# Optimization experiments

Measured on AMD Instinct MI355X. Metric: run time of the kernel, lower is better.

Reference implementation:

```python
import jax, jax.numpy as jnp
import numpy as np

B, T, E = 16, 1024, 1024
H, Dh = 16, 64


def setup_inputs() -> dict:
    key = jax.random.key(0)
    ks = jax.random.split(key, 6)
    s = 1.0 / np.sqrt(E)
    x = jax.random.normal(ks[0], (B, T, E), dtype=jnp.float32)
    Wq = jax.random.uniform(ks[1], (H, E, Dh), minval=-s, maxval=s, dtype=jnp.float32)
    Wk = jax.random.uniform(ks[2], (H, E, Dh), minval=-s, maxval=s, dtype=jnp.float32)
    Wv = jax.random.uniform(ks[3], (H, E, Dh), minval=-s, maxval=s, dtype=jnp.float32)
    sp = 1.0 / np.sqrt(H * Dh)
    Wo = jax.random.uniform(ks[4], (H * Dh, E), minval=-sp, maxval=sp, dtype=jnp.float32)
    bo = jax.random.uniform(ks[5], (E,), minval=-sp, maxval=sp, dtype=jnp.float32)
    return {"x": x, "Wq": Wq, "Wk": Wk, "Wv": Wv, "Wo": Wo, "bo": bo}


def reference(x, Wq, Wk, Wv, Wo, bo):
    # batched per-head projections: [B,T,E] x [H,E,Dh] -> [B,H,T,Dh]
    q = jnp.einsum('bte,hed->bhtd', x, Wq)
    k = jnp.einsum('bte,hed->bhtd', x, Wk)
    v = jnp.einsum('bte,hed->bhtd', x, Wv)
    scale = 1.0 / np.sqrt(Dh).astype(np.float32)
    wei = jnp.einsum('bhtd,bhsd->bhts', q, k) * scale  # [B,H,T,T]
    causal = jnp.tril(jnp.ones((T, T), dtype=bool))
    wei = jnp.where(causal, wei, -jnp.inf)
    wei = jax.nn.softmax(wei, axis=-1)
    out = jnp.einsum('bhts,bhsd->bhtd', wei, v)  # [B,H,T,Dh]
    out = out.transpose(0, 2, 1, 3).reshape(B, T, H * Dh)  # concat heads
    return out @ Wo + bo
```

## Files before the change

### kernel.cpp

```cpp
#include <hip/hip_runtime.h>
#include <stdint.h>

typedef __attribute__((ext_vector_type(8))) short short8;
typedef __attribute__((ext_vector_type(4))) float f32x4;
typedef __attribute__((ext_vector_type(4))) unsigned short u16x4;

#define DEVI static __device__ __forceinline__

DEVI unsigned short f2bf(float f) {
  unsigned int u = __builtin_bit_cast(unsigned int, f);
  u += 0x7fffu + ((u >> 16) & 1u);
  return (unsigned short)(u >> 16);
}

DEVI void glds16(const void* g, void* lds_uniform) {
  typedef const __attribute__((address_space(1))) unsigned int* gp_t;
  typedef __attribute__((address_space(3))) unsigned int* lp_t;
  __builtin_amdgcn_global_load_lds((gp_t)(uintptr_t)g, (lp_t)(uintptr_t)lds_uniform, 16, 0, 0);
}


__global__ __launch_bounds__(256) void cvt_x_kernel(const float* __restrict__ in,
                                                    unsigned short* __restrict__ out, int n4) {
  typedef __attribute__((ext_vector_type(4))) float f4;
  typedef __attribute__((ext_vector_type(4))) unsigned short u4;
  const f4* in4 = (const f4*)in;
  u4* out4 = (u4*)out;
  for (int i = blockIdx.x * blockDim.x + threadIdx.x; i < n4; i += gridDim.x * blockDim.x) {
    f4 v = in4[i];
    u4 o;
    o[0] = f2bf(v[0]); o[1] = f2bf(v[1]); o[2] = f2bf(v[2]); o[3] = f2bf(v[3]);
    out4[i] = o;
  }
}

__global__ __launch_bounds__(256) void cvt_w_kernel(const float* __restrict__ in,
                                                    unsigned short* __restrict__ out,
                                                    int total, int log2C) {
  int i = blockIdx.x * blockDim.x + threadIdx.x;
  if (i >= total) return;
  int r = i & 1023;
  int rest = i >> 10;
  int c = rest & ((1 << log2C) - 1);
  int b = rest >> log2C;
  out[i] = f2bf(in[((((size_t)b << 10) | (size_t)r) << log2C) | (size_t)c]);
}

template <int MODE>
__global__ __launch_bounds__(256)
void gemm128(const unsigned short* __restrict__ A,
             const unsigned short* __restrict__ Bt,
             unsigned short* __restrict__ OutB,
             float* __restrict__ OutF,
             const float* __restrict__ bias) {
  __shared__ unsigned short As[128 * 64];
  __shared__ unsigned short Bs[128 * 64];
  const int tid = threadIdx.x;
  const int w = tid >> 6, lane = tid & 63;
  const int l15 = lane & 15, l4 = lane >> 4;

  const int SN = (MODE == 0) ? 6 : 2;
  const int q8 = (MODE == 0) ? 384 : 128;
  const int phys = blockIdx.x;
  const int wgid = (phys & 7) * q8 + (phys >> 3);
  const int st = wgid >> 4, loc = wgid & 15;
  const int sm = st / SN, sn = st % SN;
  const int bm = (((sm << 2) + (loc >> 2)) << 7);
  const int bn = (((sn << 2) + (loc & 3)) << 7);

  f32x4 acc[4][4];
#pragma unroll
  for (int i = 0; i < 4; ++i)
#pragma unroll
    for (int j = 0; j < 4; ++j) acc[i][j] = f32x4{0.f, 0.f, 0.f, 0.f};

  const int wr = w >> 1, wc = w & 1;

  int Crow[4], Kel[4];
#pragma unroll
  for (int j = 0; j < 4; ++j) {
    int C = (((j << 2) + w) << 6) + lane;
    int row = C >> 3, cc = C & 7;
    Crow[j] = row;
    Kel[j] = ((cc ^ (row & 7)) << 3);
  }

  for (int kt = 0; kt < 16; ++kt) {
    int k0 = kt << 6;
#pragma unroll
    for (int j = 0; j < 4; ++j) {
      const unsigned short* g = A + (size_t)(bm + Crow[j]) * 1024 + k0 + Kel[j];
      glds16(g, &As[(size_t)(((j << 2) + w) << 6) * 8]);
    }
#pragma unroll
    for (int j = 0; j < 4; ++j) {
      const unsigned short* g = Bt + (size_t)(bn + Crow[j]) * 1024 + k0 + Kel[j];
      glds16(g, &Bs[(size_t)(((j << 2) + w) << 6) * 8]);
    }
    __syncthreads();
    __builtin_amdgcn_s_setprio(1);
#pragma unroll
    for (int ks = 0; ks < 2; ++ks) {
      short8 af[4], bfr[4];
#pragma unroll
      for (int mi = 0; mi < 4; ++mi) {
        int row = (wr << 6) + (mi << 4) + l15;
        int ch = ((ks << 2) + l4) ^ (row & 7);
        af[mi] = *(const short8*)&As[(row << 6) + (ch << 3)];
      }
#pragma unroll
      for (int ni = 0; ni < 4; ++ni) {
        int row = (wc << 6) + (ni << 4) + l15;
        int ch = ((ks << 2) + l4) ^ (row & 7);
        bfr[ni] = *(const short8*)&Bs[(row << 6) + (ch << 3)];
      }
#pragma unroll
      for (int mi = 0; mi < 4; ++mi)
#pragma unroll
        for (int ni = 0; ni < 4; ++ni)
          acc[mi][ni] = __builtin_amdgcn_mfma_f32_16x16x32_bf16(af[mi], bfr[ni], acc[mi][ni], 0, 0, 0);
    }
    __builtin_amdgcn_s_setprio(0);
    __syncthreads();
  }

  if (MODE == 0) {
    const int nb = bn + (wc << 6);
    const int z = nb >> 10;
    if (z < 2) {
      unsigned short* Oz = OutB + (size_t)z * 16777216;
#pragma unroll
      for (int mi = 0; mi < 4; ++mi) {
#pragma unroll
        for (int r = 0; r < 4; ++r) {
          int m = bm + (wr << 6) + (mi << 4) + (l4 << 2) + r;
          int b = m >> 10, t = m & 1023;
#pragma unroll
          for (int ni = 0; ni < 4; ++ni) {
            int n1 = (nb + (ni << 4) + l15) & 1023;
            int h = n1 >> 6, d = n1 & 63;
            Oz[((size_t)(b * 16 + h) * 1024 + t) * 64 + d] = f2bf(acc[mi][ni][r]);
          }
        }
      }
    } else {
      unsigned short* Oz = OutB + (size_t)2 * 16777216;
#pragma unroll
      for (int mi = 0; mi < 4; ++mi) {
        int tb = bm + (wr << 6) + (mi << 4) + (l4 << 2);
        int bb = tb >> 10, tt = tb & 1023;
#pragma unroll
        for (int ni = 0; ni < 4; ++ni) {
          int n1 = (nb + (ni << 4) + l15) & 1023;
          int hh = n1 >> 6, dd = n1 & 63;
          u16x4 pk;
#pragma unroll
          for (int r = 0; r < 4; ++r) pk[r] = f2bf(acc[mi][ni][r]);
          *(u16x4*)&Oz[(((size_t)((bb << 4) + hh) << 6) + (size_t)dd) * 1024 + tt] = pk;
        }
      }
    }
  } else {
#pragma unroll
    for (int mi = 0; mi < 4; ++mi) {
#pragma unroll
      for (int r = 0; r < 4; ++r) {
        int m = bm + (wr << 6) + (mi << 4) + (l4 << 2) + r;
#pragma unroll
        for (int ni = 0; ni < 4; ++ni) {
          int n = bn + (wc << 6) + (ni << 4) + l15;
          OutF[(size_t)m * 1024 + n] = acc[mi][ni][r] + bias[n];
        }
      }
    }
  }
}

__global__ __launch_bounds__(256)
void attn_fa(const unsigned short* __restrict__ Qb,
             const unsigned short* __restrict__ Kb,
             const unsigned short* __restrict__ Vtb,
             unsigned short* __restrict__ Ob) {
  __shared__ unsigned short Ks[2][64 * 64];
  __shared__ unsigned short Vs[2][64 * 64];
  __shared__ unsigned short Ps[4][16 * 64];
  const int tid = threadIdx.x, w = tid >> 6, lane = tid & 63;
  const int l15 = lane & 15, l4 = lane >> 4;
  const int phys = blockIdx.x;
  const int ord = phys >> 3;
  const int bx = ord & 7;
  const int bh = ((phys & 7) << 5) | (ord >> 3);
  const unsigned short* Q = Qb + ((size_t)bh << 16);
  const unsigned short* K = Kb + ((size_t)bh << 16);
  const unsigned short* Vt = Vtb + ((size_t)bh << 16);
  const int b = bh >> 4, h = bh & 15;
  const float SC = 0.125f * 1.44269504088896340736f;
  const float NEGINF = -__builtin_inff();

  int srow[2], skoff[2];
#pragma unroll
  for (int c = 0; c < 2; ++c) {
    int C = (c << 8) + tid;
    int row = C >> 3, cc = C & 7;
    srow[c] = row;
    skoff[c] = ((cc ^ (row & 7)) << 3);
  }
  const int sdst = (w << 6) << 3;

  for (int ph = 0; ph < 2; ++ph) {
    const int qidx = ph ? bx : (15 - bx);
    const int q0 = qidx << 6;
    const int nt = qidx + 1;
    const int qrow = q0 + (w << 4) + l15;

    short8 bq0, bq1;
    {
      const unsigned short* qp = Q + (size_t)qrow * 64 + (l4 << 3);
      bq0 = *(const short8*)qp;
      bq1 = *(const short8*)(qp + 32);
    }

    f32x4 o[4];
#pragma unroll
    for (int nf = 0; nf < 4; ++nf) o[nf] = f32x4{0.f, 0.f, 0.f, 0.f};
    float mreg = NEGINF, lreg = 0.f;

#pragma unroll
    for (int c = 0; c < 2; ++c) {
      glds16(K + (size_t)(srow[c] << 6) + skoff[c], &Ks[0][(c << 11) + sdst]);
      glds16(Vt + (size_t)(srow[c] << 10) + skoff[c], &Vs[0][(c << 11) + sdst]);
    }
    __syncthreads();

    for (int it = 0; it < nt; ++it) {
      const int cur = it & 1;
      if (it + 1 < nt) {
        const int kv0n = (it + 1) << 6;
#pragma unroll
        for (int c = 0; c < 2; ++c) {
          glds16(K + (size_t)((kv0n + srow[c]) << 6) + skoff[c], &Ks[cur ^ 1][(c << 11) + sdst]);
          glds16(Vt + (size_t)(srow[c] << 10) + kv0n + skoff[c], &Vs[cur ^ 1][(c << 11) + sdst]);
        }
      }

      f32x4 s[4];
      __builtin_amdgcn_s_setprio(1);
#pragma unroll
      for (int n = 0; n < 4; ++n) {
        const int row = (n << 4) + l15;
        const int rb = row << 6;
        short8 ak0 = *(const short8*)&Ks[cur][rb + ((l4 ^ (row & 7)) << 3)];
        short8 ak1 = *(const short8*)&Ks[cur][rb + (((4 + l4) ^ (row & 7)) << 3)];
        f32x4 a = f32x4{0.f, 0.f, 0.f, 0.f};
        a = __builtin_amdgcn_mfma_f32_16x16x32_bf16(ak0, bq0, a, 0, 0, 0);
        a = __builtin_amdgcn_mfma_f32_16x16x32_bf16(ak1, bq1, a, 0, 0, 0);
        s[n] = a;
      }
      __builtin_amdgcn_s_setprio(0);

      const int kv0 = it << 6;
      const bool diag = (it == nt - 1);
      float p[4][4];
      float mx = NEGINF;
#pragma unroll
      for (int n = 0; n < 4; ++n)
#pragma unroll
        for (int r = 0; r < 4; ++r) {
          float v = s[n][r] * SC;
          if (diag) {
            int kvg = kv0 + (n << 4) + (l4 << 2) + r;
            v = (kvg <= qrow) ? v : NEGINF;
          }
          p[n][r] = v;
          mx = fmaxf(mx, v);
        }
      mx = fmaxf(mx, __shfl_xor(mx, 16));
      mx = fmaxf(mx, __shfl_xor(mx, 32));
      float mnew = fmaxf(mreg, mx);
      float alpha = exp2f(mreg - mnew);
      mreg = mnew;
      float rs = 0.f;
#pragma unroll
      for (int n = 0; n < 4; ++n)
#pragma unroll
        for (int r = 0; r < 4; ++r) {
          float pv = exp2f(p[n][r] - mreg);
          p[n][r] = pv;
          rs += pv;
        }
      rs += __shfl_xor(rs, 16);
      rs += __shfl_xor(rs, 32);
      lreg = lreg * alpha + rs;

      float a_r[4];
#pragma unroll
      for (int r = 0; r < 4; ++r)
        a_r[r] = __shfl(alpha, (lane & 0x30) | ((l4 << 2) | r));
#pragma unroll
      for (int nf = 0; nf < 4; ++nf)
#pragma unroll
        for (int r = 0; r < 4; ++r) o[nf][r] *= a_r[r];

#pragma unroll
      for (int n = 0; n < 4; ++n) {
        u16x4 pk;
#pragma unroll
        for (int r = 0; r < 4; ++r) pk[r] = f2bf(p[n][r]);
        const int kc = (n << 1) + (l4 >> 1);
        char* addr = (char*)&Ps[w][0] + (l15 << 7) + ((kc ^ (l15 & 7)) << 4) + ((l4 & 1) << 3);
        *(u16x4*)addr = pk;
      }

      short8 pa0 = *(const short8*)((char*)&Ps[w][0] + (l15 << 7) + ((l4 ^ (l15 & 7)) << 4));
      short8 pa1 = *(const short8*)((char*)&Ps[w][0] + (l15 << 7) + (((4 + l4) ^ (l15 & 7)) << 4));
      __builtin_amdgcn_s_setprio(1);
#pragma unroll
      for (int nf = 0; nf < 4; ++nf) {
        const int drow = (nf << 4) + l15;
        const int db = drow << 6;
        short8 vb0 = *(const short8*)&Vs[cur][db + ((l4 ^ (drow & 7)) << 3)];
        short8 vb1 = *(const short8*)&Vs[cur][db + (((4 + l4) ^ (drow & 7)) << 3)];
        o[nf] = __builtin_amdgcn_mfma_f32_16x16x32_bf16(pa0, vb0, o[nf], 0, 0, 0);
        o[nf] = __builtin_amdgcn_mfma_f32_16x16x32_bf16(pa1, vb1, o[nf], 0, 0, 0);
      }
      __builtin_amdgcn_s_setprio(0);
      __syncthreads();
    }

    float linv = 1.0f / lreg;
    float l_r[4];
#pragma unroll
    for (int r = 0; r < 4; ++r)
      l_r[r] = __shfl(linv, (lane & 0x30) | ((l4 << 2) | r));
#pragma unroll
    for (int r = 0; r < 4; ++r) {
      const int t = q0 + (w << 4) + (l4 << 2) + r;
      size_t base = ((size_t)(b * 1024 + t) << 10) + (h << 6);
#pragma unroll
      for (int nf = 0; nf < 4; ++nf)
        Ob[base + (nf << 4) + l15] = f2bf(o[nf][r] * l_r[r]);
    }
  }
}


extern "C" void kernel_launch(void* const* d_in, const int* in_sizes, int n_in,
                              void* d_out, int out_size, void* d_ws, size_t ws_size,
                              hipStream_t stream) {
  const float* x  = (const float*)d_in[0];
  const float* Wq = (const float*)d_in[1];
  const float* Wk = (const float*)d_in[2];
  const float* Wv = (const float*)d_in[3];
  const float* Wo = (const float*)d_in[4];
  const float* bo = (const float*)d_in[5];
  float* out = (float*)d_out;

  unsigned char* ws = (unsigned char*)d_ws;
  unsigned short* xb  = (unsigned short*)(ws);
  unsigned short* wT  = (unsigned short*)(ws + 33554432);
  unsigned short* woT = (unsigned short*)(ws + 33554432 + 6291456);
  unsigned short* qkv = (unsigned short*)(ws + 41943040);
  unsigned short* Ob  = xb;

  cvt_x_kernel<<<2048, 256, 0, stream>>>(x, xb, 4194304);
  cvt_w_kernel<<<4096, 256, 0, stream>>>(Wq, wT,              1 << 20, 6);
  cvt_w_kernel<<<4096, 256, 0, stream>>>(Wk, wT + (1 << 20),  1 << 20, 6);
  cvt_w_kernel<<<4096, 256, 0, stream>>>(Wv, wT + (2 << 20),  1 << 20, 6);
  cvt_w_kernel<<<4096, 256, 0, stream>>>(Wo, woT,             1 << 20, 10);

  gemm128<0><<<3072, 256, 0, stream>>>(xb, wT, qkv, nullptr, nullptr);
  attn_fa<<<2048, 256, 0, stream>>>(qkv, qkv + 16777216, qkv + 33554432, Ob);
  gemm128<1><<<1024, 256, 0, stream>>>(Ob, woT, nullptr, out, bo);
}
```

Before: 418.9 us.

## Switch projection GEMMs to 256x256 tiles with double-buffered LDS pipeline

Replaces the 128x128, 256-thread GEMM with a 256x256, 512-thread kernel that double-buffers A/B tiles in LDS and overlaps the global-to-LDS load for the next k-step with MFMA compute, using explicit vmcnt waits and barriers. Each wave now computes a 128x64 sub-tile in four quadrant passes, which raises reuse per loaded byte and halves the number of workgroups. It also merges the three Q/K/V weight conversion launches into one kernel. The cost is much more LDS per block (128 KB), higher register pressure from 32 accumulators, and fewer blocks for MODE 1 (256), which may underfill the GPU.

```diff
diff --git a/kernel.cpp b/kernel.cpp
--- a/kernel.cpp
+++ b/kernel.cpp
@@ -34,6 +34,19 @@
   }
 }
 
+__global__ __launch_bounds__(256) void cvt_w3_kernel(const float* __restrict__ Wq,
+                                                     const float* __restrict__ Wk,
+                                                     const float* __restrict__ Wv,
+                                                     unsigned short* __restrict__ out) {
+  int i = blockIdx.x * blockDim.x + threadIdx.x;
+  int z = i >> 20, loc = i & 1048575;
+  const float* W = (z == 0) ? Wq : ((z == 1) ? Wk : Wv);
+  int r = loc & 1023;
+  int rest = loc >> 10;
+  int c = rest & 63, hh = rest >> 6;
+  out[i] = f2bf(W[((((size_t)hh << 10) | (size_t)r) << 6) | (size_t)c]);
+}
+
 __global__ __launch_bounds__(256) void cvt_w_kernel(const float* __restrict__ in,
                                                     unsigned short* __restrict__ out,
                                                     int total, int log2C) {
@@ -47,93 +60,115 @@
 }
 
 template <int MODE>
-__global__ __launch_bounds__(256)
-void gemm128(const unsigned short* __restrict__ A,
+__global__ __launch_bounds__(512, 2)
+void gemm256(const unsigned short* __restrict__ A,
              const unsigned short* __restrict__ Bt,
              unsigned short* __restrict__ OutB,
              float* __restrict__ OutF,
              const float* __restrict__ bias) {
-  __shared__ unsigned short As[128 * 64];
-  __shared__ unsigned short Bs[128 * 64];
+  __shared__ unsigned short As[2][256 * 64];
+  __shared__ unsigned short Bs[2][256 * 64];
   const int tid = threadIdx.x;
   const int w = tid >> 6, lane = tid & 63;
   const int l15 = lane & 15, l4 = lane >> 4;
-
-  const int SN = (MODE == 0) ? 6 : 2;
-  const int q8 = (MODE == 0) ? 384 : 128;
+  const int wm = w >> 2, wn = w & 3;
+
   const int phys = blockIdx.x;
-  const int wgid = (phys & 7) * q8 + (phys >> 3);
-  const int st = wgid >> 4, loc = wgid & 15;
-  const int sm = st / SN, sn = st % SN;
-  const int bm = (((sm << 2) + (loc >> 2)) << 7);
-  const int bn = (((sn << 2) + (loc & 3)) << 7);
-
-  f32x4 acc[4][4];
-#pragma unroll
-  for (int i = 0; i < 4; ++i)
+  const int wgid = (MODE == 0) ? ((phys & 7) * 96 + (phys >> 3))
+                               : ((phys & 7) * 32 + (phys >> 3));
+  const int sm = (MODE == 0) ? (wgid / 12) : (wgid >> 2);
+  const int sn = (MODE == 0) ? (wgid % 12) : (wgid & 3);
+  const int bm = sm << 8, bn = sn << 8;
+
+  int srow[4], skoff[4];
+#pragma unroll
+  for (int j = 0; j < 4; ++j) {
+    int C = (j << 9) + tid;
+    srow[j] = C >> 3;
+    skoff[j] = (((C & 7) ^ (srow[j] & 7)) << 3);
+  }
+
+  f32x4 acc[8][4];
+#pragma unroll
+  for (int i = 0; i < 8; ++i)
 #pragma unroll
     for (int j = 0; j < 4; ++j) acc[i][j] = f32x4{0.f, 0.f, 0.f, 0.f};
 
-  const int wr = w >> 1, wc = w & 1;
-
-  int Crow[4], Kel[4];
-#pragma unroll
-  for (int j = 0; j < 4; ++j) {
-    int C = (((j << 2) + w) << 6) + lane;
-    int row = C >> 3, cc = C & 7;
-    Crow[j] = row;
-    Kel[j] = ((cc ^ (row & 7)) << 3);
-  }
+  auto stage = [&](int buf, int kt) {
+    const int k0 = kt << 6;
+#pragma unroll
+    for (int j = 0; j < 4; ++j)
+      glds16(A + (size_t)(bm + srow[j]) * 1024 + k0 + skoff[j],
+             &As[buf][((j << 9) + (w << 6)) << 3]);
+#pragma unroll
+    for (int j = 0; j < 4; ++j)
+      glds16(Bt + (size_t)(bn + srow[j]) * 1024 + k0 + skoff[j],
+             &Bs[buf][((j << 9) + (w << 6)) << 3]);
+  };
+
+  stage(0, 0);
+  stage(1, 1);
+  asm volatile("s_waitcnt vmcnt(8)" ::: "memory");
+  __builtin_amdgcn_s_barrier();
+  __builtin_amdgcn_sched_barrier(0);
 
   for (int kt = 0; kt < 16; ++kt) {
-    int k0 = kt << 6;
-#pragma unroll
-    for (int j = 0; j < 4; ++j) {
-      const unsigned short* g = A + (size_t)(bm + Crow[j]) * 1024 + k0 + Kel[j];
-      glds16(g, &As[(size_t)(((j << 2) + w) << 6) * 8]);
-    }
-#pragma unroll
-    for (int j = 0; j < 4; ++j) {
-      const unsigned short* g = Bt + (size_t)(bn + Crow[j]) * 1024 + k0 + Kel[j];
-      glds16(g, &Bs[(size_t)(((j << 2) + w) << 6) * 8]);
-    }
-    __syncthreads();
-    __builtin_amdgcn_s_setprio(1);
-#pragma unroll
-    for (int ks = 0; ks < 2; ++ks) {
-      short8 af[4], bfr[4];
-#pragma unroll
-      for (int mi = 0; mi < 4; ++mi) {
-        int row = (wr << 6) + (mi << 4) + l15;
-        int ch = ((ks << 2) + l4) ^ (row & 7);
-        af[mi] = *(const short8*)&As[(row << 6) + (ch << 3)];
-      }
-#pragma unroll
-      for (int ni = 0; ni < 4; ++ni) {
-        int row = (wc << 6) + (ni << 4) + l15;
-        int ch = ((ks << 2) + l4) ^ (row & 7);
-        bfr[ni] = *(const short8*)&Bs[(row << 6) + (ch << 3)];
-      }
-#pragma unroll
-      for (int mi = 0; mi < 4; ++mi)
-#pragma unroll
-        for (int ni = 0; ni < 4; ++ni)
-          acc[mi][ni] = __builtin_amdgcn_mfma_f32_16x16x32_bf16(af[mi], bfr[ni], acc[mi][ni], 0, 0, 0);
-    }
-    __builtin_amdgcn_s_setprio(0);
-    __syncthreads();
+    const int cur = kt & 1;
+    if (kt >= 1) {
+      if (kt < 15) {
+        stage(cur ^ 1, kt + 1);
+        asm volatile("s_waitcnt vmcnt(8)" ::: "memory");
+      } else {
+        asm volatile("s_waitcnt vmcnt(0)" ::: "memory");
+      }
+      __builtin_amdgcn_s_barrier();
+      __builtin_amdgcn_sched_barrier(0);
+    }
+#pragma unroll
+    for (int q = 0; q < 4; ++q) {
+      const int qr = q >> 1, qc = q & 1;
+      short8 af[4][2], bfr[2][2];
+#pragma unroll
+      for (int ri = 0; ri < 4; ++ri)
+#pragma unroll
+        for (int ks = 0; ks < 2; ++ks) {
+          int row = (wm << 7) + (qr << 6) + (ri << 4) + l15;
+          int ch = ((ks << 2) + l4) ^ (row & 7);
+          af[ri][ks] = *(const short8*)&As[cur][(row << 6) + (ch << 3)];
+        }
+#pragma unroll
+      for (int ni = 0; ni < 2; ++ni)
+#pragma unroll
+        for (int ks = 0; ks < 2; ++ks) {
+          int row = (wn << 6) + (qc << 5) + (ni << 4) + l15;
+          int ch = ((ks << 2) + l4) ^ (row & 7);
+          bfr[ni][ks] = *(const short8*)&Bs[cur][(row << 6) + (ch << 3)];
+        }
+      __builtin_amdgcn_s_barrier();
+      __builtin_amdgcn_s_setprio(1);
+#pragma unroll
+      for (int ks = 0; ks < 2; ++ks)
+#pragma unroll
+        for (int ri = 0; ri < 4; ++ri)
+#pragma unroll
+          for (int ni = 0; ni < 2; ++ni)
+            acc[(qr << 2) + ri][(qc << 1) + ni] = __builtin_amdgcn_mfma_f32_16x16x32_bf16(
+                af[ri][ks], bfr[ni][ks], acc[(qr << 2) + ri][(qc << 1) + ni], 0, 0, 0);
+      __builtin_amdgcn_s_setprio(0);
+      __builtin_amdgcn_s_barrier();
+    }
   }
 
   if (MODE == 0) {
-    const int nb = bn + (wc << 6);
+    const int nb = bn + (wn << 6);
     const int z = nb >> 10;
     if (z < 2) {
       unsigned short* Oz = OutB + (size_t)z * 16777216;
 #pragma unroll
-      for (int mi = 0; mi < 4; ++mi) {
+      for (int mi = 0; mi < 8; ++mi) {
 #pragma unroll
         for (int r = 0; r < 4; ++r) {
-          int m = bm + (wr << 6) + (mi << 4) + (l4 << 2) + r;
+          int m = bm + (wm << 7) + (mi << 4) + (l4 << 2) + r;
           int b = m >> 10, t = m & 1023;
 #pragma unroll
           for (int ni = 0; ni < 4; ++ni) {
@@ -146,8 +181,8 @@
     } else {
       unsigned short* Oz = OutB + (size_t)2 * 16777216;
 #pragma unroll
-      for (int mi = 0; mi < 4; ++mi) {
-        int tb = bm + (wr << 6) + (mi << 4) + (l4 << 2);
+      for (int mi = 0; mi < 8; ++mi) {
+        int tb = bm + (wm << 7) + (mi << 4) + (l4 << 2);
         int bb = tb >> 10, tt = tb & 1023;
 #pragma unroll
         for (int ni = 0; ni < 4; ++ni) {
@@ -162,13 +197,13 @@
     }
   } else {
 #pragma unroll
-    for (int mi = 0; mi < 4; ++mi) {
+    for (int mi = 0; mi < 8; ++mi) {
 #pragma unroll
       for (int r = 0; r < 4; ++r) {
-        int m = bm + (wr << 6) + (mi << 4) + (l4 << 2) + r;
+        int m = bm + (wm << 7) + (mi << 4) + (l4 << 2) + r;
 #pragma unroll
         for (int ni = 0; ni < 4; ++ni) {
-          int n = bn + (wc << 6) + (ni << 4) + l15;
+          int n = bn + (wn << 6) + (ni << 4) + l15;
           OutF[(size_t)m * 1024 + n] = acc[mi][ni][r] + bias[n];
         }
       }
@@ -363,12 +398,10 @@
   unsigned short* Ob  = xb;
 
   cvt_x_kernel<<<2048, 256, 0, stream>>>(x, xb, 4194304);
-  cvt_w_kernel<<<4096, 256, 0, stream>>>(Wq, wT,              1 << 20, 6);
-  cvt_w_kernel<<<4096, 256, 0, stream>>>(Wk, wT + (1 << 20),  1 << 20, 6);
-  cvt_w_kernel<<<4096, 256, 0, stream>>>(Wv, wT + (2 << 20),  1 << 20, 6);
-  cvt_w_kernel<<<4096, 256, 0, stream>>>(Wo, woT,             1 << 20, 10);
-
-  gemm128<0><<<3072, 256, 0, stream>>>(xb, wT, qkv, nullptr, nullptr);
+  cvt_w3_kernel<<<12288, 256, 0, stream>>>(Wq, Wk, Wv, wT);
+  cvt_w_kernel<<<4096, 256, 0, stream>>>(Wo, woT, 1 << 20, 10);
+
+  gemm256<0><<<768, 512, 0, stream>>>(xb, wT, qkv, nullptr, nullptr);
   attn_fa<<<2048, 256, 0, stream>>>(qkv, qkv + 16777216, qkv + 33554432, Ob);
-  gemm128<1><<<1024, 256, 0, stream>>>(Ob, woT, nullptr, out, bo);
-}
+  gemm256<1><<<256, 512, 0, stream>>>(Ob, woT, nullptr, out, bo);
+}
```

Measured after the change: 419.8 us. About the same (+0.2%).
